# Performance work log

Measured on AMD Instinct MI355X. Metric: run time of the kernel, lower is better.

The kernel has to match this reference:

```python
import jax, jax.numpy as jnp
import numpy as np

D_IN = 1024
D_OUT = 1024
N_HEADS = 16

def setup_inputs() -> dict:
    key = jax.random.key(0)
    ks = jax.random.split(key, 6)
    s = 0.02
    return {
        "x": jax.random.normal(ks[0], (4, 2048, D_IN), dtype=jnp.float32),
        "Wq": jax.random.normal(ks[1], (D_IN, D_OUT), dtype=jnp.float32) * s,
        "Wk": jax.random.normal(ks[2], (D_IN, D_OUT), dtype=jnp.float32) * s,
        "Wv": jax.random.normal(ks[3], (D_IN, D_OUT), dtype=jnp.float32) * s,
        "Wo": jax.random.normal(ks[4], (D_OUT, D_OUT), dtype=jnp.float32) * s,
        "bo": jax.random.normal(ks[5], (D_OUT,), dtype=jnp.float32) * s,
    }

def reference(x, Wq, Wk, Wv, Wo, bo):
    b, n, _ = x.shape
    hd = D_OUT // N_HEADS
    # project and split heads -> [b, h, n, hd]
    def split(t):
        return t.reshape(b, n, N_HEADS, hd).transpose(0, 2, 1, 3)
    q = split(x @ Wq)
    k = split(x @ Wk)
    v = split(x @ Wv)
    scores = jnp.einsum('bhqd,bhkd->bhqk', q, k)  # [b,h,n,n]
    causal = jnp.tril(jnp.ones((n, n), dtype=bool))
    scores = jnp.where(causal, scores, -jnp.inf)
    attn = jax.nn.softmax(scores / jnp.sqrt(jnp.float32(hd)), axis=-1)
    ctx = jnp.einsum('bhqk,bhkd->bhqd', attn, v)  # [b,h,n,hd]
    ctx = ctx.transpose(0, 2, 1, 3).reshape(b, n, D_OUT)
    return ctx @ Wo + bo
```

## Files before the change

kernel.cpp:

```cpp
#include <hip/hip_runtime.h>
#include <stdint.h>

typedef unsigned short u16;
typedef __attribute__((ext_vector_type(8))) short frag8;
typedef __attribute__((ext_vector_type(4))) float f32x4;
typedef __attribute__((ext_vector_type(4))) unsigned short u16x4;
typedef __attribute__((ext_vector_type(2))) unsigned int u32x2;

#define MFMA_BF16(a,b,c) __builtin_amdgcn_mfma_f32_16x16x32_bf16((a),(b),(c),0,0,0)
#define SMSCALE 0.18033688011112042f
#define EXP2R(x) __builtin_amdgcn_exp2f(x)

__device__ __forceinline__ u16 f2bf(float f) {
  union { float f; uint32_t u; } c; c.f = f;
  uint32_t u = c.u;
  uint32_t r = (u + 0x7fffu + ((u >> 16) & 1u)) >> 16;
  return (u16)r;
}

__device__ __forceinline__ uint32_t pack_bf16(float a, float b) {
  uint32_t au = __float_as_uint(a) + 0x8000u;
  uint32_t bu = __float_as_uint(b) + 0x8000u;
  return __builtin_amdgcn_perm(bu, au, 0x07060302u);
}
__device__ __forceinline__ uint32_t pack_bf16_trunc(float a, float b) {
  return __builtin_amdgcn_perm(__float_as_uint(b), __float_as_uint(a), 0x07060302u);
}

__device__ __forceinline__ void async16(const void* g, void* l) {
  __builtin_amdgcn_global_load_lds((const __attribute__((address_space(1))) void*)g,
                                   (__attribute__((address_space(3))) void*)l,
                                   16, 0, 0);
}

__global__ __launch_bounds__(256) void k_convert_x(const float4* __restrict__ x,
                                                   u16* __restrict__ xb) {
  int i = blockIdx.x * 256 + threadIdx.x;
  float4 v = x[i];
  u16x4 o;
  o.x = f2bf(v.x); o.y = f2bf(v.y); o.z = f2bf(v.z); o.w = f2bf(v.w);
  *(u16x4*)(xb + (size_t)i * 4) = o;
}

__global__ __launch_bounds__(256) void k_transpose_w4(
    const float* __restrict__ W0, const float* __restrict__ W1,
    const float* __restrict__ W2, const float* __restrict__ W3,
    u16* __restrict__ D0, u16* __restrict__ D1,
    u16* __restrict__ D2, u16* __restrict__ D3) {
  __shared__ float tile[64][65];
  const int z = blockIdx.z;
  const float* src = (z == 0) ? W0 : (z == 1) ? W1 : (z == 2) ? W2 : W3;
  u16* dst = (z == 0) ? D0 : (z == 1) ? D1 : (z == 2) ? D2 : D3;
  const int bx = blockIdx.x * 64;
  const int by = blockIdx.y * 64;
  const int t = threadIdx.x;
  const int tc = (t & 15) * 4;
  const int tr = t >> 4;
  #pragma unroll
  for (int p = 0; p < 4; ++p) {
    int r = tr + p * 16;
    float4 v = *(const float4*)(src + (size_t)(bx + r) * 1024 + by + tc);
    tile[r][tc + 0] = v.x; tile[r][tc + 1] = v.y;
    tile[r][tc + 2] = v.z; tile[r][tc + 3] = v.w;
  }
  __syncthreads();
  #pragma unroll
  for (int p = 0; p < 4; ++p) {
    int r = tr + p * 16;
    u16x4 o;
    o.x = f2bf(tile[tc + 0][r]);
    o.y = f2bf(tile[tc + 1][r]);
    o.z = f2bf(tile[tc + 2][r]);
    o.w = f2bf(tile[tc + 3][r]);
    *(u16x4*)(dst + (size_t)(by + r) * 1024 + bx + tc) = o;
  }
}

__device__ __forceinline__ void gemm_core_256x128(
    const u16* __restrict__ Ag,
    const u16* __restrict__ Bg,
    int m0, int n0, u16* smem, f32x4 (&acc)[4][4]) {
  const int t = threadIdx.x, lane = t & 63, wv = t >> 6;
  const int lm = lane & 15, quad = lane >> 4;
  const int wr = wv >> 1, wc = wv & 1;

  const u16* sA[4]; int dA[4];
  #pragma unroll
  for (int it = 0; it < 4; ++it) {
    int chunk = it * 512 + t;
    int r = chunk >> 3;
    int sc = ((chunk & 7) ^ (r & 7)) * 8;
    sA[it] = Ag + (size_t)(m0 + r) * 1024 + sc;
    dA[it] = (it * 512 + wv * 64) * 8;
  }
  const u16* sB[2]; int dB[2];
  #pragma unroll
  for (int it = 0; it < 2; ++it) {
    int chunk = it * 512 + t;
    int r = chunk >> 3;
    int sc = ((chunk & 7) ^ (r & 7)) * 8;
    sB[it] = Bg + (size_t)(n0 + r) * 1024 + sc;
    dB[it] = 16384 + (it * 512 + wv * 64) * 8;
  }

  int offA[2][4], offB[2][4];
  #pragma unroll
  for (int kk = 0; kk < 2; ++kk) {
    #pragma unroll
    for (int i = 0; i < 4; ++i) {
      int rowa = wr * 64 + i * 16 + lm;
      offA[kk][i] = rowa * 64 + (((kk * 4 + quad) ^ (rowa & 7)) * 8);
      int rowb = wc * 64 + i * 16 + lm;
      offB[kk][i] = 16384 + rowb * 64 + (((kk * 4 + quad) ^ (rowb & 7)) * 8);
    }
  }

  #pragma unroll
  for (int it = 0; it < 4; ++it) async16(sA[it], smem + dA[it]);
  #pragma unroll
  for (int it = 0; it < 2; ++it) async16(sB[it], smem + dB[it]);
  #pragma unroll
  for (int it = 0; it < 4; ++it) async16(sA[it] + 64, smem + 24576 + dA[it]);
  #pragma unroll
  for (int it = 0; it < 2; ++it) async16(sB[it] + 64, smem + 24576 + dB[it]);
  asm volatile("s_waitcnt vmcnt(6)" ::: "memory");
  __builtin_amdgcn_s_barrier();

  int cb = 0;
  for (int tt = 0; tt < 16; ++tt) {
    u16* base = smem + cb * 24576;
    int pb = cb + 2; if (pb >= 3) pb -= 3;
    u16* pbase = smem + pb * 24576;
    const int kg = (tt + 2) * 64;
    const bool pf = (tt + 2 < 16);
    frag8 a[4], b[4];

    #pragma unroll
    for (int i = 0; i < 4; ++i) a[i] = *(const frag8*)(base + offA[0][i]);
    #pragma unroll
    for (int j = 0; j < 4; ++j) b[j] = *(const frag8*)(base + offB[0][j]);
    if (pf) {
      async16(sA[0] + kg, pbase + dA[0]);
      async16(sA[1] + kg, pbase + dA[1]);
      async16(sB[0] + kg, pbase + dB[0]);
    }
    __builtin_amdgcn_s_barrier();
    asm volatile("s_waitcnt lgkmcnt(0)" ::: "memory");
    __builtin_amdgcn_s_setprio(1);
    #pragma unroll
    for (int j = 0; j < 4; ++j)
      #pragma unroll
      for (int i = 0; i < 4; ++i)
        acc[i][j] = MFMA_BF16(a[i], b[j], acc[i][j]);
    __builtin_amdgcn_s_setprio(0);
    __builtin_amdgcn_s_barrier();

    #pragma unroll
    for (int i = 0; i < 4; ++i) a[i] = *(const frag8*)(base + offA[1][i]);
    #pragma unroll
    for (int j = 0; j < 4; ++j) b[j] = *(const frag8*)(base + offB[1][j]);
    if (pf) {
      async16(sA[2] + kg, pbase + dA[2]);
      async16(sA[3] + kg, pbase + dA[3]);
      async16(sB[1] + kg, pbase + dB[1]);
    }
    __builtin_amdgcn_s_barrier();
    asm volatile("s_waitcnt lgkmcnt(0)" ::: "memory");
    __builtin_amdgcn_s_setprio(1);
    #pragma unroll
    for (int j = 0; j < 4; ++j)
      #pragma unroll
      for (int i = 0; i < 4; ++i)
        acc[i][j] = MFMA_BF16(a[i], b[j], acc[i][j]);
    __builtin_amdgcn_s_setprio(0);
    if (pf) { asm volatile("s_waitcnt vmcnt(6)" ::: "memory"); }
    else    { asm volatile("s_waitcnt vmcnt(0)" ::: "memory"); }
    __builtin_amdgcn_s_barrier();

    cb = cb + 1; if (cb >= 3) cb = 0;
  }
}

__global__ __launch_bounds__(512, 2) void k_gemm_qkv(
    const u16* __restrict__ xb, const u16* __restrict__ Wt,
    u16* __restrict__ Qg, u16* __restrict__ Kg, u16* __restrict__ Vtg) {
  __shared__ __attribute__((aligned(16))) u16 smem[73728];
  const int bid = blockIdx.x;
  const int wgid = (bid & 7) * 96 + (bid >> 3);
  const int mt = wgid / 24, nt_ = wgid - mt * 24;
  const int m0 = mt * 256, n0 = nt_ * 128;
  f32x4 acc[4][4] = {};
  gemm_core_256x128(xb, Wt, m0, n0, smem, acc);

  const int t = threadIdx.x, lane = t & 63, wv = t >> 6;
  const int lm = lane & 15, quad = lane >> 4;
  const int wr = wv >> 1, wc = wv & 1;
  const int z = n0 >> 10, nz = n0 & 1023;

  if (z < 2) {
    u16* tgt = z ? Kg : Qg;
    const float sc = z ? 1.0f : SMSCALE;
    #pragma unroll
    for (int i = 0; i < 4; ++i)
      #pragma unroll
      for (int j = 0; j < 4; ++j) {
        const int col = nz + wc * 64 + j * 16 + lm;
        const int h = col >> 6, d = col & 63;
        #pragma unroll
        for (int reg = 0; reg < 4; ++reg) {
          const int row = m0 + wr * 64 + i * 16 + quad * 4 + reg;
          const int bb = row >> 11, nn = row & 2047;
          tgt[(((size_t)bb * 16 + h) * 2048 + nn) * 64 + d] = f2bf(acc[i][j][reg] * sc);
        }
      }
  } else {
    u16* T = smem;
    #pragma unroll
    for (int i = 0; i < 4; ++i)
      #pragma unroll
      for (int j = 0; j < 4; ++j) {
        const int rT = wc * 64 + j * 16 + lm;
        #pragma unroll
        for (int reg = 0; reg < 4; ++reg) {
          const int cT = wr * 64 + i * 16 + quad * 4 + reg;
          T[rT * 264 + cT] = f2bf(acc[i][j][reg]);
        }
      }
    __syncthreads();
    const int bb = m0 >> 11, nn0 = m0 & 2047, h0 = nz >> 6;
    #pragma unroll
    for (int p = 0; p < 8; ++p) {
      int chunk = p * 512 + t;
      int r = chunk >> 5, tk = (chunk & 31) * 8;
      frag8 v = *(const frag8*)(T + r * 264 + tk);
      *(frag8*)(Vtg + (((size_t)bb * 16 + h0 + (r >> 6)) * 64 + (r & 63)) * 2048 +
                nn0 + tk) = v;
    }
  }
}

__global__ __launch_bounds__(256, 2) void k_attn(const u16* __restrict__ Qg,
                                                 const u16* __restrict__ Kg,
                                                 const u16* __restrict__ Vtg,
                                                 u16* __restrict__ ctx) {
  __shared__ __attribute__((aligned(16))) u16 Ks[2][64 * 64];
  __shared__ __attribute__((aligned(16))) u16 Vts[2][64 * 64];
  __shared__ __attribute__((aligned(16))) u16 Ps[4 * 16 * 72];
  const int bid = blockIdx.x;
  const int ib = bid >> 6;
  const int bh = ((bid >> 3) & 7) * 8 + (bid & 7);
  const int qts[4] = {2 * ib, 2 * ib + 1, 30 - 2 * ib, 31 - 2 * ib};
  const int t = threadIdx.x, lane = t & 63, wv = t >> 6;
  const int lm = lane & 15, quad = lane >> 4;
  const int b = bh >> 4, h = bh & 15;
  u16* const PsW = Ps + wv * (16 * 72);

  frag8 aq[4][2];
  #pragma unroll
  for (int qa = 0; qa < 4; ++qa) {
    const u16* qp = Qg + ((size_t)bh * 2048 + qts[qa] * 64 + wv * 16 + lm) * 64 + quad * 8;
    aq[qa][0] = *(const frag8*)(qp);
    aq[qa][1] = *(const frag8*)(qp + 32);
  }
  f32x4 o[4][4] = {};
  float l[4] = {0.f, 0.f, 0.f, 0.f};
  const int nst = 32 - 2 * ib;

  const u16* ksrc[2]; const u16* vsrc[2];
  #pragma unroll
  for (int it = 0; it < 2; ++it) {
    int chunk = it * 256 + t;
    int r = chunk >> 3, c = chunk & 7;
    int sc = (c ^ (r & 7)) * 8;
    ksrc[it] = Kg  + ((size_t)bh * 2048 + r) * 64 + sc;
    vsrc[it] = Vtg + ((size_t)bh * 64 + r) * 2048 + sc;
  }
  int offs[8];
  #pragma unroll
  for (int x = 0; x < 4; ++x)
    #pragma unroll
    for (int y = 0; y < 2; ++y)
      offs[x * 2 + y] = (x * 16 + lm) * 64 + (((y * 4 + quad) ^ (lm & 7)) * 8);

  auto stage = [&](int kt, int buf) {
    #pragma unroll
    for (int it = 0; it < 2; ++it) {
      async16(ksrc[it] + (size_t)kt * 4096, &Ks[buf][(it * 256 + wv * 64) * 8]);
      async16(vsrc[it] + (size_t)kt * 64,   &Vts[buf][(it * 256 + wv * 64) * 8]);
    }
  };

  stage(0, 0);
  for (int kt0 = 0; kt0 < nst; ++kt0) {
    const int cur = kt0 & 1;
    __syncthreads();
    if (kt0 + 1 < nst) stage(kt0 + 1, cur ^ 1);

    frag8 kf[8];
    #pragma unroll
    for (int i = 0; i < 8; ++i) kf[i] = *(const frag8*)(&Ks[cur][offs[i]]);

    uint32_t pk[4][8];
    #pragma unroll
    for (int qa = 0; qa < 4; ++qa) {
      if (qts[qa] < kt0) continue;
      f32x4 s[4];
      #pragma unroll
      for (int kt = 0; kt < 4; ++kt) {
        f32x4 z = {0.f, 0.f, 0.f, 0.f};
        z = MFMA_BF16(kf[kt * 2 + 0], aq[qa][0], z);
        z = MFMA_BF16(kf[kt * 2 + 1], aq[qa][1], z);
        s[kt] = z;
      }
      if (kt0 == qts[qa]) {
        #pragma unroll
        for (int kt = 0; kt < 4; ++kt)
          #pragma unroll
          for (int rg = 0; rg < 4; ++rg)
            if (kt * 16 + quad * 4 + rg > wv * 16 + lm) s[kt][rg] = -3.0e38f;
      }
      float rs = 0.f;
      #pragma unroll
      for (int kt = 0; kt < 4; ++kt) {
        float p0 = EXP2R(s[kt][0]);
        float p1 = EXP2R(s[kt][1]);
        float p2 = EXP2R(s[kt][2]);
        float p3 = EXP2R(s[kt][3]);
        rs += (p0 + p1) + (p2 + p3);
        pk[qa][kt * 2 + 0] = pack_bf16_trunc(p0, p1);
        pk[qa][kt * 2 + 1] = pack_bf16_trunc(p2, p3);
      }
      l[qa] += rs;
    }

    frag8 vf[8];
    #pragma unroll
    for (int i = 0; i < 8; ++i) vf[i] = *(const frag8*)(&Vts[cur][offs[i]]);

    #pragma unroll
    for (int qa = 0; qa < 4; ++qa) {
      if (qts[qa] < kt0) continue;
      #pragma unroll
      for (int kt = 0; kt < 4; ++kt) {
        u32x2 w; w.x = pk[qa][kt * 2 + 0]; w.y = pk[qa][kt * 2 + 1];
        *(u32x2*)(PsW + lm * 72 + kt * 16 + quad * 4) = w;
      }
      #pragma unroll
      for (int ks = 0; ks < 2; ++ks) {
        frag8 bp = *(const frag8*)(PsW + lm * 72 + ks * 32 + quad * 8);
        #pragma unroll
        for (int dt = 0; dt < 4; ++dt)
          o[qa][dt] = MFMA_BF16(vf[dt * 2 + ks], bp, o[qa][dt]);
      }
    }
  }

  #pragma unroll
  for (int qa = 0; qa < 4; ++qa) {
    float lv = l[qa];
    lv += __shfl_xor(lv, 16);
    lv += __shfl_xor(lv, 32);
    const float inv = 1.0f / lv;
    #pragma unroll
    for (int dt = 0; dt < 4; ++dt) {
      *(uint32_t*)(PsW + lm * 72 + dt * 16 + quad * 4)     = pack_bf16(o[qa][dt][0] * inv, o[qa][dt][1] * inv);
      *(uint32_t*)(PsW + lm * 72 + dt * 16 + quad * 4 + 2) = pack_bf16(o[qa][dt][2] * inv, o[qa][dt][3] * inv);
    }
    const int rr = lane >> 2, cc = (lane & 3) * 8;
    const size_t row = (size_t)b * 2048 + qts[qa] * 64 + wv * 16 + rr;
    #pragma unroll
    for (int half = 0; half < 2; ++half) {
      frag8 vo = *(const frag8*)(PsW + rr * 72 + cc + half * 32);
      *(frag8*)(ctx + row * 1024 + h * 64 + cc + half * 32) = vo;
    }
  }
}

__global__ __launch_bounds__(512, 2) void k_gemm_out(
    const u16* __restrict__ ctx, const u16* __restrict__ Wot,
    const float* __restrict__ bo, float* __restrict__ out) {
  __shared__ __attribute__((aligned(16))) u16 smem[73728];
  const int bid = blockIdx.x;
  const int wgid = (bid & 7) * 32 + (bid >> 3);
  const int m0 = (wgid >> 3) * 256, n0 = (wgid & 7) * 128;
  f32x4 acc[4][4] = {};
  gemm_core_256x128(ctx, Wot, m0, n0, smem, acc);

  const int t = threadIdx.x, lane = t & 63, wv = t >> 6;
  const int lm = lane & 15, quad = lane >> 4;
  const int wr = wv >> 1, wc = wv & 1;
  #pragma unroll
  for (int i = 0; i < 4; ++i)
    #pragma unroll
    for (int j = 0; j < 4; ++j) {
      const int col = n0 + wc * 64 + j * 16 + lm;
      const float bias = bo[col];
      #pragma unroll
      for (int reg = 0; reg < 4; ++reg) {
        const int row = m0 + wr * 64 + i * 16 + quad * 4 + reg;
        out[(size_t)row * 1024 + col] = acc[i][j][reg] + bias;
      }
    }
}

extern "C" void kernel_launch(void* const* d_in, const int* in_sizes, int n_in,
                              void* d_out, int out_size, void* d_ws, size_t ws_size,
                              hipStream_t stream) {
  const float* x  = (const float*)d_in[0];
  const float* Wq = (const float*)d_in[1];
  const float* Wk = (const float*)d_in[2];
  const float* Wv = (const float*)d_in[3];
  const float* Wo = (const float*)d_in[4];
  const float* bo = (const float*)d_in[5];
  float* out = (float*)d_out;
  char* ws = (char*)d_ws;

  u16* xb   = (u16*)(ws);
  u16* Wqt  = (u16*)(ws + ((size_t)16 << 20));
  u16* Wkt  = (u16*)(ws + ((size_t)18 << 20));
  u16* Wvt  = (u16*)(ws + ((size_t)20 << 20));
  u16* Wot  = (u16*)(ws + ((size_t)22 << 20));
  u16* Qg   = (u16*)(ws + ((size_t)24 << 20));
  u16* Kg   = (u16*)(ws + ((size_t)40 << 20));
  u16* Vtg  = (u16*)(ws + ((size_t)56 << 20));
  u16* ctxb = (u16*)(ws + ((size_t)72 << 20));

  k_convert_x<<<8192, 256, 0, stream>>>((const float4*)x, xb);
  k_transpose_w4<<<dim3(16, 16, 4), 256, 0, stream>>>(Wq, Wk, Wv, Wo, Wqt, Wkt, Wvt, Wot);
  k_gemm_qkv<<<768, 512, 0, stream>>>(xb, Wqt, Qg, Kg, Vtg);
  k_attn<<<512, 256, 0, stream>>>(Qg, Kg, Vtg, ctxb);
  k_gemm_out<<<256, 512, 0, stream>>>(ctxb, Wot, bo, out);
}
```

Baseline: 244.4 us.

## Template GEMM core with K-step 32 and retile QKV and output GEMMs

Replaces the fixed 256x128, K-step-64 GEMM core with a templated core that uses a K-step of 32 and a configurable block tile and wave layout. The QKV projection now uses 128x256 tiles computed by 4 waves, each covering 128x64. The output projection uses 128x128 tiles across 512 blocks, allowing 3 blocks per CU. The goal is a smaller LDS footprint and more blocks in flight, to improve occupancy and load balance. In exchange it runs twice as many pipeline iterations and barriers, and it drops the XOR swizzle on shared memory, which may add LDS bank conflicts.

```diff
diff --git a/kernel.cpp b/kernel.cpp
--- a/kernel.cpp
+++ b/kernel.cpp
@@ -76,104 +76,97 @@
   }
 }
 
-__device__ __forceinline__ void gemm_core_256x128(
+template<int BM, int BN, int WM, int WN>
+__device__ __forceinline__ void gemm_core32(
     const u16* __restrict__ Ag,
     const u16* __restrict__ Bg,
-    int m0, int n0, u16* smem, f32x4 (&acc)[4][4]) {
+    int m0, int n0, u16* smem,
+    f32x4 (&acc)[BM / (WM * 16)][BN / (WN * 16)]) {
+  constexpr int WAVES = WM * WN;
+  constexpr int MF = BM / (WM * 16), NF = BN / (WN * 16);
+  constexpr int AI = BM / 16 / WAVES;
+  constexpr int BI = BN / 16 / WAVES;
+  constexpr int L  = AI + BI;
+  constexpr int L0 = (L + 1) / 2;
+  constexpr int TILE = (BM + BN) * 32;
+  constexpr int BOFF = BM * 32;
   const int t = threadIdx.x, lane = t & 63, wv = t >> 6;
   const int lm = lane & 15, quad = lane >> 4;
-  const int wr = wv >> 1, wc = wv & 1;
-
-  const u16* sA[4]; int dA[4];
-  #pragma unroll
-  for (int it = 0; it < 4; ++it) {
-    int chunk = it * 512 + t;
-    int r = chunk >> 3;
-    int sc = ((chunk & 7) ^ (r & 7)) * 8;
-    sA[it] = Ag + (size_t)(m0 + r) * 1024 + sc;
-    dA[it] = (it * 512 + wv * 64) * 8;
-  }
-  const u16* sB[2]; int dB[2];
-  #pragma unroll
-  for (int it = 0; it < 2; ++it) {
-    int chunk = it * 512 + t;
-    int r = chunk >> 3;
-    int sc = ((chunk & 7) ^ (r & 7)) * 8;
-    sB[it] = Bg + (size_t)(n0 + r) * 1024 + sc;
-    dB[it] = 16384 + (it * 512 + wv * 64) * 8;
-  }
-
-  int offA[2][4], offB[2][4];
-  #pragma unroll
-  for (int kk = 0; kk < 2; ++kk) {
-    #pragma unroll
-    for (int i = 0; i < 4; ++i) {
-      int rowa = wr * 64 + i * 16 + lm;
-      offA[kk][i] = rowa * 64 + (((kk * 4 + quad) ^ (rowa & 7)) * 8);
-      int rowb = wc * 64 + i * 16 + lm;
-      offB[kk][i] = 16384 + rowb * 64 + (((kk * 4 + quad) ^ (rowb & 7)) * 8);
-    }
-  }
-
-  #pragma unroll
-  for (int it = 0; it < 4; ++it) async16(sA[it], smem + dA[it]);
-  #pragma unroll
-  for (int it = 0; it < 2; ++it) async16(sB[it], smem + dB[it]);
-  #pragma unroll
-  for (int it = 0; it < 4; ++it) async16(sA[it] + 64, smem + 24576 + dA[it]);
-  #pragma unroll
-  for (int it = 0; it < 2; ++it) async16(sB[it] + 64, smem + 24576 + dB[it]);
-  asm volatile("s_waitcnt vmcnt(6)" ::: "memory");
+  const int wr = wv / WN, wc = wv % WN;
+
+  const u16* srcs[L];
+  int dsts[L];
+  #pragma unroll
+  for (int i = 0; i < AI; ++i) {
+    int w = wv * AI + i;
+    int chunk = w * 64 + lane;
+    srcs[i] = Ag + (size_t)(m0 + (chunk >> 2)) * 1024 + (chunk & 3) * 8;
+    dsts[i] = w * 512;
+  }
+  #pragma unroll
+  for (int i = 0; i < BI; ++i) {
+    int w = wv * BI + i;
+    int chunk = w * 64 + lane;
+    srcs[AI + i] = Bg + (size_t)(n0 + (chunk >> 2)) * 1024 + (chunk & 3) * 8;
+    dsts[AI + i] = BOFF + w * 512;
+  }
+  int offA[MF], offB[NF];
+  #pragma unroll
+  for (int i = 0; i < MF; ++i) offA[i] = (wr * (BM / WM) + i * 16 + lm) * 32 + quad * 8;
+  #pragma unroll
+  for (int j = 0; j < NF; ++j) offB[j] = BOFF + (wc * (BN / WN) + j * 16 + lm) * 32 + quad * 8;
+
+  #pragma unroll
+  for (int i = 0; i < L; ++i) async16(srcs[i], smem + dsts[i]);
+  #pragma unroll
+  for (int i = 0; i < L; ++i) async16(srcs[i] + 32, smem + TILE + dsts[i]);
+  asm volatile("s_waitcnt vmcnt(%0)" :: "n"(L) : "memory");
   __builtin_amdgcn_s_barrier();
 
   int cb = 0;
-  for (int tt = 0; tt < 16; ++tt) {
-    u16* base = smem + cb * 24576;
+  for (int tt = 0; tt < 32; ++tt) {
+    u16* base = smem + cb * TILE;
     int pb = cb + 2; if (pb >= 3) pb -= 3;
-    u16* pbase = smem + pb * 24576;
-    const int kg = (tt + 2) * 64;
-    const bool pf = (tt + 2 < 16);
-    frag8 a[4], b[4];
-
-    #pragma unroll
-    for (int i = 0; i < 4; ++i) a[i] = *(const frag8*)(base + offA[0][i]);
-    #pragma unroll
-    for (int j = 0; j < 4; ++j) b[j] = *(const frag8*)(base + offB[0][j]);
+    u16* pbase = smem + pb * TILE;
+    const int kadv = (tt + 2) * 32;
+    const bool pf = (tt + 2 < 32);
+    frag8 a[MF], b[NF];
+
+    #pragma unroll
+    for (int i = 0; i < MF / 2; ++i) a[i] = *(const frag8*)(base + offA[i]);
+    #pragma unroll
+    for (int j = 0; j < NF; ++j) b[j] = *(const frag8*)(base + offB[j]);
     if (pf) {
-      async16(sA[0] + kg, pbase + dA[0]);
-      async16(sA[1] + kg, pbase + dA[1]);
-      async16(sB[0] + kg, pbase + dB[0]);
+      #pragma unroll
+      for (int i = 0; i < L0; ++i) async16(srcs[i] + kadv, pbase + dsts[i]);
     }
     __builtin_amdgcn_s_barrier();
     asm volatile("s_waitcnt lgkmcnt(0)" ::: "memory");
     __builtin_amdgcn_s_setprio(1);
     #pragma unroll
-    for (int j = 0; j < 4; ++j)
-      #pragma unroll
-      for (int i = 0; i < 4; ++i)
+    for (int j = 0; j < NF; ++j)
+      #pragma unroll
+      for (int i = 0; i < MF / 2; ++i)
         acc[i][j] = MFMA_BF16(a[i], b[j], acc[i][j]);
     __builtin_amdgcn_s_setprio(0);
     __builtin_amdgcn_s_barrier();
 
     #pragma unroll
-    for (int i = 0; i < 4; ++i) a[i] = *(const frag8*)(base + offA[1][i]);
-    #pragma unroll
-    for (int j = 0; j < 4; ++j) b[j] = *(const frag8*)(base + offB[1][j]);
+    for (int i = MF / 2; i < MF; ++i) a[i] = *(const frag8*)(base + offA[i]);
     if (pf) {
-      async16(sA[2] + kg, pbase + dA[2]);
-      async16(sA[3] + kg, pbase + dA[3]);
-      async16(sB[1] + kg, pbase + dB[1]);
+      #pragma unroll
+      for (int i = L0; i < L; ++i) async16(srcs[i] + kadv, pbase + dsts[i]);
     }
     __builtin_amdgcn_s_barrier();
     asm volatile("s_waitcnt lgkmcnt(0)" ::: "memory");
     __builtin_amdgcn_s_setprio(1);
     #pragma unroll
-    for (int j = 0; j < 4; ++j)
-      #pragma unroll
-      for (int i = 0; i < 4; ++i)
+    for (int j = 0; j < NF; ++j)
+      #pragma unroll
+      for (int i = MF / 2; i < MF; ++i)
         acc[i][j] = MFMA_BF16(a[i], b[j], acc[i][j]);
     __builtin_amdgcn_s_setprio(0);
-    if (pf) { asm volatile("s_waitcnt vmcnt(6)" ::: "memory"); }
+    if (pf) { asm volatile("s_waitcnt vmcnt(%0)" :: "n"(L) : "memory"); }
     else    { asm volatile("s_waitcnt vmcnt(0)" ::: "memory"); }
     __builtin_amdgcn_s_barrier();
 
@@ -181,34 +174,34 @@
   }
 }
 
-__global__ __launch_bounds__(512, 2) void k_gemm_qkv(
+__global__ __launch_bounds__(256, 2) void k_gemm_qkv(
     const u16* __restrict__ xb, const u16* __restrict__ Wt,
     u16* __restrict__ Qg, u16* __restrict__ Kg, u16* __restrict__ Vtg) {
-  __shared__ __attribute__((aligned(16))) u16 smem[73728];
+  __shared__ __attribute__((aligned(16))) u16 smem[3 * (128 + 256) * 32];
   const int bid = blockIdx.x;
   const int wgid = (bid & 7) * 96 + (bid >> 3);
-  const int mt = wgid / 24, nt_ = wgid - mt * 24;
-  const int m0 = mt * 256, n0 = nt_ * 128;
-  f32x4 acc[4][4] = {};
-  gemm_core_256x128(xb, Wt, m0, n0, smem, acc);
+  const int mt = wgid & 63, nt = wgid >> 6;
+  const int m0 = mt * 128, n0g = nt * 256;
+  f32x4 acc[8][4] = {};
+  gemm_core32<128, 256, 1, 4>(xb, Wt, m0, n0g, smem, acc);
 
   const int t = threadIdx.x, lane = t & 63, wv = t >> 6;
   const int lm = lane & 15, quad = lane >> 4;
-  const int wr = wv >> 1, wc = wv & 1;
-  const int z = n0 >> 10, nz = n0 & 1023;
+  const int wc = wv & 3;
+  const int z = n0g >> 10, nz = n0g & 1023;
 
   if (z < 2) {
     u16* tgt = z ? Kg : Qg;
     const float sc = z ? 1.0f : SMSCALE;
     #pragma unroll
-    for (int i = 0; i < 4; ++i)
+    for (int i = 0; i < 8; ++i)
       #pragma unroll
       for (int j = 0; j < 4; ++j) {
         const int col = nz + wc * 64 + j * 16 + lm;
         const int h = col >> 6, d = col & 63;
         #pragma unroll
         for (int reg = 0; reg < 4; ++reg) {
-          const int row = m0 + wr * 64 + i * 16 + quad * 4 + reg;
+          const int row = m0 + i * 16 + quad * 4 + reg;
           const int bb = row >> 11, nn = row & 2047;
           tgt[(((size_t)bb * 16 + h) * 2048 + nn) * 64 + d] = f2bf(acc[i][j][reg] * sc);
         }
@@ -216,24 +209,25 @@
   } else {
     u16* T = smem;
     #pragma unroll
-    for (int i = 0; i < 4; ++i)
+    for (int i = 0; i < 8; ++i)
       #pragma unroll
       for (int j = 0; j < 4; ++j) {
         const int rT = wc * 64 + j * 16 + lm;
         #pragma unroll
         for (int reg = 0; reg < 4; ++reg) {
-          const int cT = wr * 64 + i * 16 + quad * 4 + reg;
-          T[rT * 264 + cT] = f2bf(acc[i][j][reg]);
+          const int cT = i * 16 + quad * 4 + reg;
+          T[rT * 136 + cT] = f2bf(acc[i][j][reg]);
         }
       }
     __syncthreads();
-    const int bb = m0 >> 11, nn0 = m0 & 2047, h0 = nz >> 6;
-    #pragma unroll
-    for (int p = 0; p < 8; ++p) {
-      int chunk = p * 512 + t;
-      int r = chunk >> 5, tk = (chunk & 31) * 8;
-      frag8 v = *(const frag8*)(T + r * 264 + tk);
-      *(frag8*)(Vtg + (((size_t)bb * 16 + h0 + (r >> 6)) * 64 + (r & 63)) * 2048 +
+    const int bb = m0 >> 11, nn0 = m0 & 2047;
+    #pragma unroll
+    for (int p = 0; p < 16; ++p) {
+      int chunk = p * 256 + t;
+      int rT = chunk >> 4, tk = (chunk & 15) * 8;
+      frag8 v = *(const frag8*)(T + rT * 136 + tk);
+      const int col = nz + rT;
+      *(frag8*)(Vtg + (((size_t)bb * 16 + (col >> 6)) * 64 + (col & 63)) * 2048 +
                 nn0 + tk) = v;
     }
   }
@@ -376,15 +370,16 @@
   }
 }
 
-__global__ __launch_bounds__(512, 2) void k_gemm_out(
+__global__ __launch_bounds__(256, 3) void k_gemm_out(
     const u16* __restrict__ ctx, const u16* __restrict__ Wot,
     const float* __restrict__ bo, float* __restrict__ out) {
-  __shared__ __attribute__((aligned(16))) u16 smem[73728];
+  __shared__ __attribute__((aligned(16))) u16 smem[3 * (128 + 128) * 32];
   const int bid = blockIdx.x;
-  const int wgid = (bid & 7) * 32 + (bid >> 3);
-  const int m0 = (wgid >> 3) * 256, n0 = (wgid & 7) * 128;
+  const int wgid = (bid & 7) * 64 + (bid >> 3);
+  const int mt = wgid & 63, nt = wgid >> 6;
+  const int m0 = mt * 128, n0 = nt * 128;
   f32x4 acc[4][4] = {};
-  gemm_core_256x128(ctx, Wot, m0, n0, smem, acc);
+  gemm_core32<128, 128, 2, 2>(ctx, Wot, m0, n0, smem, acc);
 
   const int t = threadIdx.x, lane = t & 63, wv = t >> 6;
   const int lm = lane & 15, quad = lane >> 4;
@@ -427,7 +422,7 @@
 
   k_convert_x<<<8192, 256, 0, stream>>>((const float4*)x, xb);
   k_transpose_w4<<<dim3(16, 16, 4), 256, 0, stream>>>(Wq, Wk, Wv, Wo, Wqt, Wkt, Wvt, Wot);
-  k_gemm_qkv<<<768, 512, 0, stream>>>(xb, Wqt, Qg, Kg, Vtg);
+  k_gemm_qkv<<<768, 256, 0, stream>>>(xb, Wqt, Qg, Kg, Vtg);
   k_attn<<<512, 256, 0, stream>>>(Qg, Kg, Vtg, ctxb);
-  k_gemm_out<<<256, 512, 0, stream>>>(ctxb, Wot, bo, out);
-}
+  k_gemm_out<<<512, 256, 0, stream>>>(ctxb, Wot, bo, out);
+}
```

Result: faster. 235.4 us (-3.7%).
